# Performance work log

Measured on AMD Instinct MI355X. Metric: run time of the kernel, lower is better.

## Reference

```python
import jax, jax.numpy as jnp
import numpy as np

N = 10000      # nodes
E = 320000     # edges
D = 256        # input_nf = output_nf
H = 256        # hidden_nf
ED = 16        # edges_in_d
NORM = 32.0    # normalization_factor


def setup_inputs() -> dict:
    key = jax.random.key(0)
    ks = jax.random.split(key, 16)
    s = 0.02  # param scale
    return {
        "h": jax.random.normal(ks[0], (N, D), dtype=jnp.float32),
        "edge_index": jax.random.randint(ks[1], (2, E), 0, N, dtype=jnp.int64),
        "edge_attr": jax.random.normal(ks[2], (E, ED), dtype=jnp.float32),
        "node_mask": jnp.ones((N, 1), dtype=jnp.float32),
        "edge_mask": jnp.ones((E, 1), dtype=jnp.float32),
        # edge_mlp: Linear(2D+ED -> H), SiLU, Linear(H -> H), SiLU
        "We1": jax.random.normal(ks[3], (2 * D + ED, H), dtype=jnp.float32) * s,
        "be1": jnp.zeros((H,), dtype=jnp.float32),
        "We2": jax.random.normal(ks[4], (H, H), dtype=jnp.float32) * s,
        "be2": jnp.zeros((H,), dtype=jnp.float32),
        # att_mlp: Linear(H -> 1), Sigmoid
        "Wa": jax.random.normal(ks[5], (H, 1), dtype=jnp.float32) * s,
        "ba": jnp.zeros((1,), dtype=jnp.float32),
        # node_mlp: Linear(H + D -> H), SiLU, Linear(H -> D)
        "Wn1": jax.random.normal(ks[6], (H + D, H), dtype=jnp.float32) * s,
        "bn1": jnp.zeros((H,), dtype=jnp.float32),
        "Wn2": jax.random.normal(ks[7], (H, D), dtype=jnp.float32) * s,
        "bn2": jnp.zeros((D,), dtype=jnp.float32),
    }


def reference(h, edge_index, edge_attr, node_mask, edge_mask,
              We1, be1, We2, be2, Wa, ba, Wn1, bn1, Wn2, bn2):
    row, col = edge_index[0], edge_index[1]
    # edge model: gather endpoints, concat with edge_attr -> [E, 2D+ED]
    e_in = jnp.concatenate([h[row], h[col], edge_attr], axis=1)
    mij = jax.nn.silu(jax.nn.silu(e_in @ We1 + be1) @ We2 + be2)  # [E, H]
    att = jax.nn.sigmoid(mij @ Wa + ba)                            # [E, 1]
    edge_feat = mij * att * edge_mask                              # [E, H]
    # node model: scatter-add messages to rows, normalize by constant
    agg = jax.ops.segment_sum(edge_feat, row, num_segments=h.shape[0]) / NORM  # [N, H]
    a = jnp.concatenate([h, agg], axis=1)                          # [N, D+H]
    h_out = h + (jax.nn.silu(a @ Wn1 + bn1) @ Wn2 + bn2)           # residual
    h_out = h_out * node_mask
    return (h_out, mij)
```

## Files before the change

kernel.cpp:

```cpp
#include <hip/hip_runtime.h>

#define NN 10000
#define NE 320000

typedef __bf16 bf16x8 __attribute__((ext_vector_type(8)));
typedef short  s16x8  __attribute__((ext_vector_type(8)));
typedef float  f32x4  __attribute__((ext_vector_type(4)));

__device__ __forceinline__ unsigned short f2bf(float f) {
  unsigned u = __builtin_bit_cast(unsigned, f);
  u = (u + 0x7FFFu + ((u >> 16) & 1u)) >> 16;
  return (unsigned short)u;
}
__device__ __forceinline__ float bf2f(unsigned short s) {
  unsigned u = ((unsigned)s) << 16;
  return __builtin_bit_cast(float, u);
}
__device__ __forceinline__ float sigm(float x) { return 1.0f / (1.0f + __expf(-x)); }
__device__ __forceinline__ float silu_f(float x) { return x / (1.0f + __expf(-x)); }

__global__ void prep_w(const float* __restrict__ We1, const float* __restrict__ We2,
                       const float* __restrict__ Wn1, const float* __restrict__ Wn2,
                       unsigned short* __restrict__ W1abT, unsigned short* __restrict__ W1cT,
                       unsigned short* __restrict__ We2T,
                       unsigned short* __restrict__ Wn1T, unsigned short* __restrict__ Wn2T) {
  int g = blockIdx.x * blockDim.x + threadIdx.x;
  const int S1 = 512 * 256, S2 = 256 * 32, S3 = 256 * 256, S4 = 256 * 512, S5 = 256 * 256;
  if (g < S1) {
    int n = g >> 8, k = g & 255;
    float v = (n < 256) ? We1[k * 256 + n] : We1[(256 + k) * 256 + (n - 256)];
    W1abT[g] = f2bf(v);
  } else if (g < S1 + S2) {
    int i = g - S1; int n = i >> 5, kk = i & 31;
    float v = (kk < 16) ? We1[(512 + kk) * 256 + n] : 0.0f;
    W1cT[i] = f2bf(v);
  } else if (g < S1 + S2 + S3) {
    int i = g - S1 - S2; int n = i >> 8, k = i & 255;
    We2T[i] = f2bf(We2[k * 256 + n]);
  } else if (g < S1 + S2 + S3 + S4) {
    int i = g - S1 - S2 - S3; int n = i >> 9, k = i & 511;
    Wn1T[i] = f2bf(Wn1[k * 256 + n]);
  } else if (g < S1 + S2 + S3 + S4 + S5) {
    int i = g - S1 - S2 - S3 - S4; int n = i >> 8, k = i & 255;
    Wn2T[i] = f2bf(Wn2[k * 256 + n]);
  }
}

__global__ void prep_x(const float* __restrict__ h, const float* __restrict__ eattr,
                       unsigned short* __restrict__ hb, unsigned short* __restrict__ eb) {
  int g = blockIdx.x * blockDim.x + threadIdx.x;
  const int GH = NN * 64;
  const int GE = NE * 4;
  if (g < GH) {
    float4 f = ((const float4*)h)[g];
    unsigned short* d = hb + g * 4;
    d[0] = f2bf(f.x); d[1] = f2bf(f.y); d[2] = f2bf(f.z); d[3] = f2bf(f.w);
  } else if (g < GH + GE) {
    int i = g - GH;
    float4 f = ((const float4*)eattr)[i];
    unsigned short* d = eb + i * 4;
    d[0] = f2bf(f.x); d[1] = f2bf(f.y); d[2] = f2bf(f.z); d[3] = f2bf(f.w);
  }
}

__global__ void hist_kernel(const int* __restrict__ eidx, int* __restrict__ rowi,
                            int* __restrict__ counts) {
  __shared__ int s64;
  if (threadIdx.x == 0) {
    bool b = true;
    for (int i = 1; i < 64; i += 2) b = b && (eidx[i] == 0);
    s64 = b ? 1 : 0;
  }
  __syncthreads();
  int e = blockIdx.x * 256 + threadIdx.x;
  if (e < NE) {
    int r = s64 ? (int)((const long long*)eidx)[e] : eidx[e];
    rowi[e] = r;
    atomicAdd(&counts[r], 1);
  }
}

__global__ __launch_bounds__(1024) void scan_kernel(const int* __restrict__ counts,
                                                    int* __restrict__ rowStart,
                                                    int* __restrict__ cursor) {
  __shared__ int part[1024];
  int t = threadIdx.x;
  int local[10];
  int s = 0;
  #pragma unroll
  for (int i = 0; i < 10; i++) {
    int idx = t * 10 + i;
    int c = (idx < NN) ? counts[idx] : 0;
    local[i] = s; s += c;
  }
  part[t] = s;
  __syncthreads();
  int val = s;
  for (int off = 1; off < 1024; off <<= 1) {
    int tmp = (t >= off) ? part[t - off] : 0;
    __syncthreads();
    part[t] += tmp;
    __syncthreads();
  }
  int base = part[t] - val;
  #pragma unroll
  for (int i = 0; i < 10; i++) {
    int idx = t * 10 + i;
    if (idx < NN) { int v = base + local[i]; rowStart[idx] = v; cursor[idx] = v; }
  }
  if (t == 1023) rowStart[NN] = NE;
}

__global__ void scatter_kernel(const int* __restrict__ rowi, int* __restrict__ cursor,
                               int* __restrict__ eorder) {
  int e = blockIdx.x * 256 + threadIdx.x;
  if (e < NE) {
    int pos = atomicAdd(&cursor[rowi[e]], 1);
    eorder[pos] = e;
  }
}

__global__ __launch_bounds__(512) void hpq_kernel(
    const unsigned short* __restrict__ hb, const unsigned short* __restrict__ W1abT,
    unsigned short* __restrict__ hPQb) {
  __shared__ unsigned short Abuf[128 * 40];
  __shared__ unsigned short Bbuf[256 * 40];

  const int tid = threadIdx.x;
  const int lane = tid & 63;
  const int wid = tid >> 6;
  const int wrr = wid >> 2, wcc = wid & 3;
  const int n0 = blockIdx.x * 128;
  const int coh = blockIdx.y;
  const unsigned short* Bsrc = W1abT + ((size_t)(coh << 8)) * 256;

  f32x4 acc[4][4];
  #pragma unroll
  for (int m = 0; m < 4; m++)
    #pragma unroll
    for (int n = 0; n < 4; n++) acc[m][n] = (f32x4){0.f, 0.f, 0.f, 0.f};

  const int eA = tid >> 2, sA = tid & 3;
  int nodeA = n0 + eA; if (nodeA >= NN) nodeA = NN - 1;
  const int rbase = (wrr << 6) + (lane & 15);
  const int koff = (lane >> 4) << 3;
  const int cfrag = lane & 15;

  for (int kt = 0; kt < 8; ++kt) {
    const int k0 = kt << 5;
    __syncthreads();
    *(s16x8*)&Abuf[eA * 40 + (sA << 3)] = *(const s16x8*)(hb + (size_t)nodeA * 256 + k0 + (sA << 3));
    #pragma unroll
    for (int i = 0; i < 2; ++i) {
      int idx = tid + (i << 9);
      int n = idx >> 2, s = idx & 3;
      *(s16x8*)&Bbuf[n * 40 + (s << 3)] = *(const s16x8*)(Bsrc + (n << 8) + k0 + (s << 3));
    }
    __syncthreads();
    bf16x8 a[4], b[4];
    #pragma unroll
    for (int m = 0; m < 4; m++)
      a[m] = __builtin_bit_cast(bf16x8, *(const s16x8*)&Abuf[(rbase + m * 16) * 40 + koff]);
    #pragma unroll
    for (int n = 0; n < 4; n++)
      b[n] = __builtin_bit_cast(bf16x8, *(const s16x8*)&Bbuf[((wcc << 6) + n * 16 + cfrag) * 40 + koff]);
    #pragma unroll
    for (int m = 0; m < 4; m++)
      #pragma unroll
      for (int n = 0; n < 4; n++)
        acc[m][n] = __builtin_amdgcn_mfma_f32_16x16x32_bf16(a[m], b[n], acc[m][n], 0, 0, 0);
  }

  #pragma unroll
  for (int m = 0; m < 4; m++) {
    int rl = (wrr << 6) + m * 16 + ((lane >> 4) << 2);
    #pragma unroll
    for (int n = 0; n < 4; n++) {
      int cg = (wcc << 6) + n * 16 + cfrag;
      #pragma unroll
      for (int j = 0; j < 4; j++) {
        int rg = n0 + rl + j;
        if (rg < NN) hPQb[(size_t)rg * 512 + (coh << 8) + cg] = f2bf(acc[m][n][j]);
      }
    }
  }
}

__global__ __launch_bounds__(512) void edge_kernel(
    const unsigned short* __restrict__ hPQb, const int* __restrict__ eidx,
    const unsigned short* __restrict__ eb, const float* __restrict__ emask,
    const unsigned short* __restrict__ W1cT, const float* __restrict__ be1,
    const unsigned short* __restrict__ We2T, const float* __restrict__ be2,
    const float* __restrict__ Wa, const float* __restrict__ ba,
    float* __restrict__ mij_out, float* __restrict__ attm) {
  __shared__ unsigned short Bbuf[2][256 * 40];
  __shared__ unsigned short A2[64 * 264];
  __shared__ float attP[4][64];
  __shared__ int rowL[64], colL[64];
  __shared__ float waL[256], be1L[256], be2L[256];
  __shared__ int s64;

  const int tid = threadIdx.x;
  const int lane = tid & 63;
  const int wid = tid >> 6;
  const int wr = wid >> 2, wc = wid & 3;
  const int e0 = blockIdx.x * 64;
  const int cfrag = lane & 15;
  const int lq = lane >> 4;
  const int koff = lq << 3;
  const int rbase = (wr << 5) + cfrag;

  if (tid == 0) {
    bool b = true;
    for (int i = 1; i < 64; i += 2) b = b && (eidx[i] == 0);
    s64 = b ? 1 : 0;
  }
  __syncthreads();

  if (tid < 64) {
    if (s64) {
      const long long* p64 = (const long long*)eidx;
      rowL[tid] = (int)p64[e0 + tid];
      colL[tid] = (int)p64[NE + e0 + tid];
    } else {
      rowL[tid] = eidx[e0 + tid];
      colL[tid] = eidx[NE + e0 + tid];
    }
  }
  if (tid >= 256) {
    int i = tid - 256;
    waL[i] = Wa[i]; be1L[i] = be1[i]; be2L[i] = be2[i];
  }
  __syncthreads();

  {
    int e = tid >> 3, p = tid & 7;
    int c0 = p << 5;
    const unsigned short* pr = hPQb + (size_t)rowL[e] * 512 + c0;
    const unsigned short* pc = hPQb + (size_t)colL[e] * 512 + 256 + c0;
    #pragma unroll
    for (int q = 0; q < 4; ++q) {
      s16x8 vr = *(const s16x8*)(pr + (q << 3));
      s16x8 vc = *(const s16x8*)(pc + (q << 3));
      s16x8 vo;
      #pragma unroll
      for (int j = 0; j < 8; ++j)
        vo[j] = (short)f2bf(bf2f((unsigned short)vr[j]) + bf2f((unsigned short)vc[j]));
      *(s16x8*)&A2[e * 264 + c0 + (q << 3)] = vo;
    }
  }

  const int sn0 = tid >> 2;
  const int ss0 = (tid & 3) << 3;
  {
    s16x8 v0 = *(const s16x8*)(W1cT + sn0 * 32 + ss0);
    s16x8 v1 = *(const s16x8*)(W1cT + (sn0 + 128) * 32 + ss0);
    *(s16x8*)&Bbuf[0][sn0 * 40 + ss0] = v0;
    *(s16x8*)&Bbuf[0][(sn0 + 128) * 40 + ss0] = v1;
  }
  __syncthreads();

  f32x4 acc[2][4];
  #pragma unroll
  for (int m = 0; m < 2; m++)
    #pragma unroll
    for (int n = 0; n < 4; n++) acc[m][n] = (f32x4){0.f, 0.f, 0.f, 0.f};

  for (int t = 0; t < 9; ++t) {
    const int cur = t & 1, nxt = cur ^ 1;

    s16x8 nb0, nb1;
    const bool doStage = (t < 8);
    if (doStage) {
      const int k0 = t << 5;
      nb0 = *(const s16x8*)(We2T + (sn0 << 8) + k0 + ss0);
      nb1 = *(const s16x8*)(We2T + ((sn0 + 128) << 8) + k0 + ss0);
    }

    bf16x8 a[2];
    if (t == 0) {
      #pragma unroll
      for (int m = 0; m < 2; m++) {
        int rl = rbase + m * 16;
        if (koff < 16)
          a[m] = __builtin_bit_cast(bf16x8, *(const s16x8*)(eb + (size_t)(e0 + rl) * 16 + koff));
        else
          a[m] = __builtin_bit_cast(bf16x8, (s16x8){0, 0, 0, 0, 0, 0, 0, 0});
      }
    } else {
      const int k0 = (t - 1) << 5;
      #pragma unroll
      for (int m = 0; m < 2; m++)
        a[m] = __builtin_bit_cast(bf16x8, *(const s16x8*)&A2[(rbase + m * 16) * 264 + k0 + koff]);
    }

    bf16x8 b[4];
    #pragma unroll
    for (int n = 0; n < 4; n++)
      b[n] = __builtin_bit_cast(bf16x8, *(const s16x8*)&Bbuf[cur][((wc << 6) + n * 16 + cfrag) * 40 + koff]);

    #pragma unroll
    for (int m = 0; m < 2; m++)
      #pragma unroll
      for (int n = 0; n < 4; n++)
        acc[m][n] = __builtin_amdgcn_mfma_f32_16x16x32_bf16(a[m], b[n], acc[m][n], 0, 0, 0);

    if (doStage) {
      *(s16x8*)&Bbuf[nxt][sn0 * 40 + ss0] = nb0;
      *(s16x8*)&Bbuf[nxt][(sn0 + 128) * 40 + ss0] = nb1;
    }

    if (t == 0) {
      #pragma unroll
      for (int m = 0; m < 2; m++) {
        int rl = (wr << 5) + m * 16 + (lq << 2);
        #pragma unroll
        for (int n = 0; n < 4; n++) {
          int cg = (wc << 6) + n * 16 + cfrag;
          float bias = be1L[cg];
          #pragma unroll
          for (int j = 0; j < 4; j++) {
            float x = acc[m][n][j] + bf2f(A2[(rl + j) * 264 + cg]) + bias;
            A2[(rl + j) * 264 + cg] = f2bf(silu_f(x));
          }
          acc[m][n] = (f32x4){0.f, 0.f, 0.f, 0.f};
        }
      }
    }
    __syncthreads();
  }

  float part[2][4];
  #pragma unroll
  for (int m = 0; m < 2; m++)
    #pragma unroll
    for (int j = 0; j < 4; j++) part[m][j] = 0.f;

  #pragma unroll
  for (int m = 0; m < 2; m++) {
    #pragma unroll
    for (int n = 0; n < 4; n++) {
      int cg = (wc << 6) + n * 16 + cfrag;
      float bias = be2L[cg];
      float wav = waL[cg];
      #pragma unroll
      for (int j = 0; j < 4; j++) {
        int row = (wr << 5) + m * 16 + (lq << 2) + j;
        float x = silu_f(acc[m][n][j] + bias);
        mij_out[(size_t)(e0 + row) * 256 + cg] = x;
        part[m][j] += x * wav;
      }
    }
  }
  #pragma unroll
  for (int m = 0; m < 2; m++)
    #pragma unroll
    for (int j = 0; j < 4; j++) {
      float p = part[m][j];
      p += __shfl_xor(p, 1);
      p += __shfl_xor(p, 2);
      p += __shfl_xor(p, 4);
      p += __shfl_xor(p, 8);
      part[m][j] = p;
    }
  if (cfrag == 0) {
    #pragma unroll
    for (int m = 0; m < 2; m++)
      #pragma unroll
      for (int j = 0; j < 4; j++)
        attP[wc][(wr << 5) + m * 16 + (lq << 2) + j] = part[m][j];
  }
  __syncthreads();
  if (tid < 64) {
    float s = attP[0][tid] + attP[1][tid] + attP[2][tid] + attP[3][tid] + ba[0];
    attm[e0 + tid] = sigm(s) * emask[e0 + tid];
  }
}

__global__ __launch_bounds__(256) void agg_kernel(
    const float* __restrict__ mij, const float* __restrict__ attm,
    const int* __restrict__ rowStart, const int* __restrict__ eorder,
    float* __restrict__ agg) {
  int n = blockIdx.x;
  int t = threadIdx.x;
  int start = rowStart[n], end = rowStart[n + 1];
  float s = 0.f;
  int i = start;
  for (; i + 4 <= end; i += 4) {
    int ea = eorder[i], eb = eorder[i + 1], ec = eorder[i + 2], ed = eorder[i + 3];
    float aa = attm[ea], ab = attm[eb], ac = attm[ec], ad = attm[ed];
    s += mij[(size_t)ea * 256 + t] * aa;
    s += mij[(size_t)eb * 256 + t] * ab;
    s += mij[(size_t)ec * 256 + t] * ac;
    s += mij[(size_t)ed * 256 + t] * ad;
  }
  for (; i < end; ++i) {
    int e = eorder[i];
    s += mij[(size_t)e * 256 + t] * attm[e];
  }
  agg[(size_t)n * 256 + t] = s;
}

__global__ __launch_bounds__(512) void node_kernel(
    const float* __restrict__ h, const float* __restrict__ agg,
    const float* __restrict__ nmask,
    const unsigned short* __restrict__ Wn1T, const float* __restrict__ bn1,
    const unsigned short* __restrict__ Wn2T, const float* __restrict__ bn2,
    float* __restrict__ hout) {
  __shared__ unsigned short Abuf[128 * 40];
  __shared__ unsigned short Bbuf[256 * 40];
  __shared__ unsigned short A2[128 * 264];
  __shared__ float bn1L[256], bn2L[256];

  const int tid = threadIdx.x;
  const int lane = tid & 63;
  const int wid = tid >> 6;
  const int n0 = blockIdx.x * 128;

  if (tid < 256) { bn1L[tid] = bn1[tid]; bn2L[tid] = bn2[tid]; }

  f32x4 acc[4][4];
  #pragma unroll
  for (int m = 0; m < 4; m++)
    #pragma unroll
    for (int n = 0; n < 4; n++) acc[m][n] = (f32x4){0.f, 0.f, 0.f, 0.f};

  const int eA = tid >> 2, sA = tid & 3;
  int nodeA = n0 + eA; if (nodeA >= NN) nodeA = NN - 1;
  const int wrr = wid >> 2, wcc = wid & 3;
  const int rbase = (wrr << 6) + (lane & 15);
  const int koff = (lane >> 4) << 3;
  const int cfrag = lane & 15;

  for (int kt = 0; kt < 16; ++kt) {
    const int k0 = kt << 5;
    __syncthreads();
    {
      const float* src = (k0 < 256) ? (h + (size_t)nodeA * 256 + k0 + (sA << 3))
                                    : (agg + (size_t)nodeA * 256 + (k0 - 256) + (sA << 3));
      const float sc = (k0 < 256) ? 1.0f : (1.0f / 32.0f);
      float4 f0 = *(const float4*)src;
      float4 f1 = *(const float4*)(src + 4);
      s16x8 v;
      v[0] = (short)f2bf(f0.x * sc); v[1] = (short)f2bf(f0.y * sc);
      v[2] = (short)f2bf(f0.z * sc); v[3] = (short)f2bf(f0.w * sc);
      v[4] = (short)f2bf(f1.x * sc); v[5] = (short)f2bf(f1.y * sc);
      v[6] = (short)f2bf(f1.z * sc); v[7] = (short)f2bf(f1.w * sc);
      *(s16x8*)&Abuf[eA * 40 + (sA << 3)] = v;
    }
    #pragma unroll
    for (int i = 0; i < 2; ++i) {
      int idx = tid + (i << 9);
      int n = idx >> 2, s = idx & 3;
      s16x8 v = *(const s16x8*)(Wn1T + (n << 9) + k0 + (s << 3));
      *(s16x8*)&Bbuf[n * 40 + (s << 3)] = v;
    }
    __syncthreads();
    bf16x8 a[4], b[4];
    #pragma unroll
    for (int m = 0; m < 4; m++)
      a[m] = __builtin_bit_cast(bf16x8, *(const s16x8*)&Abuf[(rbase + m * 16) * 40 + koff]);
    #pragma unroll
    for (int n = 0; n < 4; n++)
      b[n] = __builtin_bit_cast(bf16x8, *(const s16x8*)&Bbuf[((wcc << 6) + n * 16 + cfrag) * 40 + koff]);
    #pragma unroll
    for (int m = 0; m < 4; m++)
      #pragma unroll
      for (int n = 0; n < 4; n++)
        acc[m][n] = __builtin_amdgcn_mfma_f32_16x16x32_bf16(a[m], b[n], acc[m][n], 0, 0, 0);
  }

  #pragma unroll
  for (int m = 0; m < 4; m++) {
    int rl = (wrr << 6) + m * 16 + ((lane >> 4) << 2);
    #pragma unroll
    for (int n = 0; n < 4; n++) {
      int cg = (wcc << 6) + n * 16 + cfrag;
      float bias = bn1L[cg];
      #pragma unroll
      for (int j = 0; j < 4; j++) {
        float x = acc[m][n][j] + bias;
        A2[(rl + j) * 264 + cg] = f2bf(silu_f(x));
      }
      acc[m][n] = (f32x4){0.f, 0.f, 0.f, 0.f};
    }
  }

  for (int kt = 0; kt < 8; ++kt) {
    const int k0 = kt << 5;
    __syncthreads();
    #pragma unroll
    for (int i = 0; i < 2; ++i) {
      int idx = tid + (i << 9);
      int n = idx >> 2, s = idx & 3;
      s16x8 v = *(const s16x8*)(Wn2T + (n << 8) + k0 + (s << 3));
      *(s16x8*)&Bbuf[n * 40 + (s << 3)] = v;
    }
    __syncthreads();
    bf16x8 a[4], b[4];
    #pragma unroll
    for (int m = 0; m < 4; m++)
      a[m] = __builtin_bit_cast(bf16x8, *(const s16x8*)&A2[(rbase + m * 16) * 264 + k0 + koff]);
    #pragma unroll
    for (int n = 0; n < 4; n++)
      b[n] = __builtin_bit_cast(bf16x8, *(const s16x8*)&Bbuf[((wcc << 6) + n * 16 + cfrag) * 40 + koff]);
    #pragma unroll
    for (int m = 0; m < 4; m++)
      #pragma unroll
      for (int n = 0; n < 4; n++)
        acc[m][n] = __builtin_amdgcn_mfma_f32_16x16x32_bf16(a[m], b[n], acc[m][n], 0, 0, 0);
  }

  #pragma unroll
  for (int m = 0; m < 4; m++) {
    int rl = (wrr << 6) + m * 16 + ((lane >> 4) << 2);
    #pragma unroll
    for (int n = 0; n < 4; n++) {
      int cg = (wcc << 6) + n * 16 + cfrag;
      #pragma unroll
      for (int j = 0; j < 4; j++) {
        int rg = n0 + rl + j;
        if (rg < NN) {
          float val = acc[m][n][j] + bn2L[cg];
          float o = (h[(size_t)rg * 256 + cg] + val) * nmask[rg];
          hout[(size_t)rg * 256 + cg] = o;
        }
      }
    }
  }
}

extern "C" void kernel_launch(void* const* d_in, const int* in_sizes, int n_in,
                              void* d_out, int out_size, void* d_ws, size_t ws_size,
                              hipStream_t stream) {
  (void)in_sizes; (void)n_in; (void)out_size; (void)ws_size;
  const float* h     = (const float*)d_in[0];
  const int*   eidx  = (const int*)d_in[1];
  const float* eattr = (const float*)d_in[2];
  const float* nmask = (const float*)d_in[3];
  const float* emask = (const float*)d_in[4];
  const float* We1 = (const float*)d_in[5];
  const float* be1 = (const float*)d_in[6];
  const float* We2 = (const float*)d_in[7];
  const float* be2 = (const float*)d_in[8];
  const float* Wa  = (const float*)d_in[9];
  const float* ba  = (const float*)d_in[10];
  const float* Wn1 = (const float*)d_in[11];
  const float* bn1 = (const float*)d_in[12];
  const float* Wn2 = (const float*)d_in[13];
  const float* bn2 = (const float*)d_in[14];

  char* ws = (char*)d_ws;
  unsigned short* W1abT = (unsigned short*)(ws + 0);
  unsigned short* W1cT  = (unsigned short*)(ws + 262144);
  unsigned short* We2T  = (unsigned short*)(ws + 278528);
  unsigned short* Wn1T  = (unsigned short*)(ws + 409600);
  unsigned short* Wn2T  = (unsigned short*)(ws + 671744);
  float*          agg   = (float*)(ws + 802816);
  unsigned short* hPQb  = (unsigned short*)(ws + 802816);
  float* attm     = (float*)(ws + 11042816);
  int*   counts   = (int*)(ws + 12322816);
  int*   rowStart = (int*)(ws + 12362816);
  int*   cursor   = (int*)(ws + 12402824);
  int*   eorder   = (int*)(ws + 12442824);
  int*   rowi     = (int*)(ws + 13722824);
  unsigned short* hb  = (unsigned short*)(ws + 15003008);
  unsigned short* ebf = (unsigned short*)(ws + 20123008);

  float* hout = (float*)d_out;
  float* mij  = (float*)d_out + (size_t)NN * 256;

  hipMemsetAsync(counts, 0, NN * sizeof(int), stream);
  prep_w<<<1568, 256, 0, stream>>>(We1, We2, Wn1, Wn2, W1abT, W1cT, We2T, Wn1T, Wn2T);
  prep_x<<<7500, 256, 0, stream>>>(h, eattr, hb, ebf);
  hist_kernel<<<(NE + 255) / 256, 256, 0, stream>>>(eidx, rowi, counts);
  scan_kernel<<<1, 1024, 0, stream>>>(counts, rowStart, cursor);
  scatter_kernel<<<(NE + 255) / 256, 256, 0, stream>>>(rowi, cursor, eorder);
  hpq_kernel<<<dim3((NN + 127) / 128, 2), 512, 0, stream>>>(hb, W1abT, hPQb);
  edge_kernel<<<NE / 64, 512, 0, stream>>>(hPQb, eidx, ebf, emask, W1cT, be1, We2T, be2,
                                           Wa, ba, mij, attm);
  agg_kernel<<<NN, 256, 0, stream>>>(mij, attm, rowStart, eorder, agg);
  node_kernel<<<(NN + 127) / 128, 512, 0, stream>>>(h, agg, nmask, Wn1T, bn1, Wn2T, bn2, hout);
}
```

Before: 397.7 us.

## Fuse segment-sum aggregation into edge kernel using row-sorted edge order

Edges are now processed in row-sorted order, so each 64-edge block computes attention-weighted messages and reduces runs of equal rows in shared memory. Interior rows are written directly and boundary rows are added atomically, which removes the separate agg kernel and its re-read of the full mij tensor. Edge attributes are converted to bf16 inside the edge kernel instead of in a separate prep pass, and f2bf now uses the hardware conversion. The trade-offs are scattered mij writes and col/eattr gathers by original edge id, an extra memset of agg, and an aggregation that now sums bf16-rounded messages.

After: 371.3 us. 6.6% less time.

```diff
diff --git a/kernel.cpp b/kernel.cpp
--- a/kernel.cpp
+++ b/kernel.cpp
@@ -8,9 +8,7 @@
 typedef float  f32x4  __attribute__((ext_vector_type(4)));
 
 __device__ __forceinline__ unsigned short f2bf(float f) {
-  unsigned u = __builtin_bit_cast(unsigned, f);
-  u = (u + 0x7FFFu + ((u >> 16) & 1u)) >> 16;
-  return (unsigned short)u;
+  return __builtin_bit_cast(unsigned short, (__bf16)f);
 }
 __device__ __forceinline__ float bf2f(unsigned short s) {
   unsigned u = ((unsigned)s) << 16;
@@ -46,19 +44,11 @@
   }
 }
 
-__global__ void prep_x(const float* __restrict__ h, const float* __restrict__ eattr,
-                       unsigned short* __restrict__ hb, unsigned short* __restrict__ eb) {
+__global__ void prep_x(const float* __restrict__ h, unsigned short* __restrict__ hb) {
   int g = blockIdx.x * blockDim.x + threadIdx.x;
-  const int GH = NN * 64;
-  const int GE = NE * 4;
-  if (g < GH) {
+  if (g < NN * 64) {
     float4 f = ((const float4*)h)[g];
     unsigned short* d = hb + g * 4;
-    d[0] = f2bf(f.x); d[1] = f2bf(f.y); d[2] = f2bf(f.z); d[3] = f2bf(f.w);
-  } else if (g < GH + GE) {
-    int i = g - GH;
-    float4 f = ((const float4*)eattr)[i];
-    unsigned short* d = eb + i * 4;
     d[0] = f2bf(f.x); d[1] = f2bf(f.y); d[2] = f2bf(f.z); d[3] = f2bf(f.w);
   }
 }
@@ -112,11 +102,13 @@
 }
 
 __global__ void scatter_kernel(const int* __restrict__ rowi, int* __restrict__ cursor,
-                               int* __restrict__ eorder) {
+                               int* __restrict__ eorder, int* __restrict__ rowSorted) {
   int e = blockIdx.x * 256 + threadIdx.x;
   if (e < NE) {
-    int pos = atomicAdd(&cursor[rowi[e]], 1);
+    int r = rowi[e];
+    int pos = atomicAdd(&cursor[r], 1);
     eorder[pos] = e;
+    rowSorted[pos] = r;
   }
 }
 
@@ -188,15 +180,17 @@
 
 __global__ __launch_bounds__(512) void edge_kernel(
     const unsigned short* __restrict__ hPQb, const int* __restrict__ eidx,
-    const unsigned short* __restrict__ eb, const float* __restrict__ emask,
+    const float* __restrict__ eattr, const float* __restrict__ emask,
     const unsigned short* __restrict__ W1cT, const float* __restrict__ be1,
     const unsigned short* __restrict__ We2T, const float* __restrict__ be2,
     const float* __restrict__ Wa, const float* __restrict__ ba,
-    float* __restrict__ mij_out, float* __restrict__ attm) {
+    const int* __restrict__ eorder, const int* __restrict__ rowSorted,
+    float* __restrict__ mij_out, float* __restrict__ agg) {
   __shared__ unsigned short Bbuf[2][256 * 40];
   __shared__ unsigned short A2[64 * 264];
   __shared__ float attP[4][64];
-  __shared__ int rowL[64], colL[64];
+  __shared__ float attL[64];
+  __shared__ int rowL[64], colL[64], origL[64];
   __shared__ float waL[256], be1L[256], be2L[256];
   __shared__ int s64;
 
@@ -218,14 +212,10 @@
   __syncthreads();
 
   if (tid < 64) {
-    if (s64) {
-      const long long* p64 = (const long long*)eidx;
-      rowL[tid] = (int)p64[e0 + tid];
-      colL[tid] = (int)p64[NE + e0 + tid];
-    } else {
-      rowL[tid] = eidx[e0 + tid];
-      colL[tid] = eidx[NE + e0 + tid];
-    }
+    int orig = eorder[e0 + tid];
+    origL[tid] = orig;
+    rowL[tid] = rowSorted[e0 + tid];
+    colL[tid] = s64 ? (int)((const long long*)eidx)[NE + orig] : eidx[NE + orig];
   }
   if (tid >= 256) {
     int i = tid - 256;
@@ -282,10 +272,19 @@
       #pragma unroll
       for (int m = 0; m < 2; m++) {
         int rl = rbase + m * 16;
-        if (koff < 16)
-          a[m] = __builtin_bit_cast(bf16x8, *(const s16x8*)(eb + (size_t)(e0 + rl) * 16 + koff));
-        else
+        if (koff < 16) {
+          const float* src = eattr + (size_t)origL[rl] * 16 + koff;
+          float4 f0 = *(const float4*)src;
+          float4 f1 = *(const float4*)(src + 4);
+          s16x8 v;
+          v[0] = (short)f2bf(f0.x); v[1] = (short)f2bf(f0.y);
+          v[2] = (short)f2bf(f0.z); v[3] = (short)f2bf(f0.w);
+          v[4] = (short)f2bf(f1.x); v[5] = (short)f2bf(f1.y);
+          v[6] = (short)f2bf(f1.z); v[7] = (short)f2bf(f1.w);
+          a[m] = __builtin_bit_cast(bf16x8, v);
+        } else {
           a[m] = __builtin_bit_cast(bf16x8, (s16x8){0, 0, 0, 0, 0, 0, 0, 0});
+        }
       }
     } else {
       const int k0 = (t - 1) << 5;
@@ -347,7 +346,8 @@
       for (int j = 0; j < 4; j++) {
         int row = (wr << 5) + m * 16 + (lq << 2) + j;
         float x = silu_f(acc[m][n][j] + bias);
-        mij_out[(size_t)(e0 + row) * 256 + cg] = x;
+        mij_out[(size_t)origL[row] * 256 + cg] = x;
+        A2[row * 264 + cg] = f2bf(x);
         part[m][j] += x * wav;
       }
     }
@@ -373,32 +373,27 @@
   __syncthreads();
   if (tid < 64) {
     float s = attP[0][tid] + attP[1][tid] + attP[2][tid] + attP[3][tid] + ba[0];
-    attm[e0 + tid] = sigm(s) * emask[e0 + tid];
-  }
-}
-
-__global__ __launch_bounds__(256) void agg_kernel(
-    const float* __restrict__ mij, const float* __restrict__ attm,
-    const int* __restrict__ rowStart, const int* __restrict__ eorder,
-    float* __restrict__ agg) {
-  int n = blockIdx.x;
-  int t = threadIdx.x;
-  int start = rowStart[n], end = rowStart[n + 1];
-  float s = 0.f;
-  int i = start;
-  for (; i + 4 <= end; i += 4) {
-    int ea = eorder[i], eb = eorder[i + 1], ec = eorder[i + 2], ed = eorder[i + 3];
-    float aa = attm[ea], ab = attm[eb], ac = attm[ec], ad = attm[ed];
-    s += mij[(size_t)ea * 256 + t] * aa;
-    s += mij[(size_t)eb * 256 + t] * ab;
-    s += mij[(size_t)ec * 256 + t] * ac;
-    s += mij[(size_t)ed * 256 + t] * ad;
-  }
-  for (; i < end; ++i) {
-    int e = eorder[i];
-    s += mij[(size_t)e * 256 + t] * attm[e];
-  }
-  agg[(size_t)n * 256 + t] = s;
+    attL[tid] = sigm(s) * emask[origL[tid]];
+  }
+  __syncthreads();
+
+  if (tid < 256) {
+    const int c = tid;
+    const int fd = rowL[0], ld = rowL[63];
+    float acc2 = 0.f;
+    int prev = fd;
+    for (int i = 0; i < 64; ++i) {
+      int r = rowL[i];
+      if (r != prev) {
+        if (prev == fd) atomicAdd(&agg[(size_t)prev * 256 + c], acc2);
+        else            agg[(size_t)prev * 256 + c] = acc2;
+        acc2 = 0.f; prev = r;
+      }
+      acc2 += attL[i] * bf2f(A2[i * 264 + c]);
+    }
+    atomicAdd(&agg[(size_t)prev * 256 + c], acc2);
+    (void)ld;
+  }
 }
 
 __global__ __launch_bounds__(512) void node_kernel(
@@ -556,29 +551,28 @@
   unsigned short* We2T  = (unsigned short*)(ws + 278528);
   unsigned short* Wn1T  = (unsigned short*)(ws + 409600);
   unsigned short* Wn2T  = (unsigned short*)(ws + 671744);
-  float*          agg   = (float*)(ws + 802816);
   unsigned short* hPQb  = (unsigned short*)(ws + 802816);
-  float* attm     = (float*)(ws + 11042816);
-  int*   counts   = (int*)(ws + 12322816);
-  int*   rowStart = (int*)(ws + 12362816);
-  int*   cursor   = (int*)(ws + 12402824);
-  int*   eorder   = (int*)(ws + 12442824);
-  int*   rowi     = (int*)(ws + 13722824);
-  unsigned short* hb  = (unsigned short*)(ws + 15003008);
-  unsigned short* ebf = (unsigned short*)(ws + 20123008);
+  float* agg      = (float*)(ws + 11042816);
+  int*   counts   = (int*)(ws + 21282816);
+  int*   rowStart = (int*)(ws + 21322816);
+  int*   cursor   = (int*)(ws + 21362824);
+  int*   eorder   = (int*)(ws + 21402824);
+  int*   rowi     = (int*)(ws + 22682824);
+  int*   rowSorted= (int*)(ws + 23962824);
+  unsigned short* hb = (unsigned short*)(ws + 25242824);
 
   float* hout = (float*)d_out;
   float* mij  = (float*)d_out + (size_t)NN * 256;
 
   hipMemsetAsync(counts, 0, NN * sizeof(int), stream);
+  hipMemsetAsync(agg, 0, (size_t)NN * 256 * sizeof(float), stream);
   prep_w<<<1568, 256, 0, stream>>>(We1, We2, Wn1, Wn2, W1abT, W1cT, We2T, Wn1T, Wn2T);
-  prep_x<<<7500, 256, 0, stream>>>(h, eattr, hb, ebf);
+  prep_x<<<2500, 256, 0, stream>>>(h, hb);
   hist_kernel<<<(NE + 255) / 256, 256, 0, stream>>>(eidx, rowi, counts);
   scan_kernel<<<1, 1024, 0, stream>>>(counts, rowStart, cursor);
-  scatter_kernel<<<(NE + 255) / 256, 256, 0, stream>>>(rowi, cursor, eorder);
+  scatter_kernel<<<(NE + 255) / 256, 256, 0, stream>>>(rowi, cursor, eorder, rowSorted);
   hpq_kernel<<<dim3((NN + 127) / 128, 2), 512, 0, stream>>>(hb, W1abT, hPQb);
-  edge_kernel<<<NE / 64, 512, 0, stream>>>(hPQb, eidx, ebf, emask, W1cT, be1, We2T, be2,
-                                           Wa, ba, mij, attm);
-  agg_kernel<<<NN, 256, 0, stream>>>(mij, attm, rowStart, eorder, agg);
+  edge_kernel<<<NE / 64, 512, 0, stream>>>(hPQb, eidx, eattr, emask, W1cT, be1, We2T, be2,
+                                           Wa, ba, eorder, rowSorted, mij, agg);
   node_kernel<<<(NN + 127) / 128, 512, 0, stream>>>(h, agg, nmask, Wn1T, bn1, Wn2T, bn2, hout);
 }
```
